# Kernel tuning notes

Measured on AMD Instinct MI355X. Metric: run time of the kernel, lower is better.

Reference implementation:

```python
import jax, jax.numpy as jnp
import numpy as np

B, T, C = 2, 1024, 2048
NH, NKV = 16, 4
HD = C // NH          # 128
NUM_REP = NH // NKV   # 4


def _apply_rotation(x, angles):
    # x: (B, T, nh, hd); angles: (T, hd//2). Equivalent to the per-pair 2x2
    # rotation matmuls in the torch code: [x0', x1'] = [[cos,-sin],[sin,cos]] @ [x0, x1]
    Bx, Tx, nh, hd = x.shape
    xp = x.reshape(Bx, Tx, nh, hd // 2, 2)
    cos = jnp.cos(angles)[None, :, None, :]  # (1, T, 1, hd//2)
    sin = jnp.sin(angles)[None, :, None, :]
    x0, x1 = xp[..., 0], xp[..., 1]
    rot = jnp.stack([cos * x0 - sin * x1, sin * x0 + cos * x1], axis=-1)
    return rot.reshape(Bx, Tx, nh, hd)


def setup_inputs() -> dict:
    key = jax.random.key(0)
    ks = jax.random.split(key, 5)
    x = jax.random.normal(ks[0], (B, T, C), dtype=jnp.float32)
    # standard RoPE angle table: pos * 10000^(-2i/hd), shape (T, hd//2)
    inv_freq = 1.0 / (10000.0 ** (jnp.arange(0, HD, 2, dtype=jnp.float32) / HD))
    angles = jnp.arange(T, dtype=jnp.float32)[:, None] * inv_freq[None, :]
    s = 0.02
    wq = jax.random.normal(ks[1], (C, C), dtype=jnp.float32) * s
    wk = jax.random.normal(ks[2], (C, NKV * HD), dtype=jnp.float32) * s
    wv = jax.random.normal(ks[3], (C, NKV * HD), dtype=jnp.float32) * s
    wo = jax.random.normal(ks[4], (C, C), dtype=jnp.float32) * s
    return {"x": x, "angles": angles, "wq": wq, "wk": wk, "wv": wv, "wo": wo}


def reference(x, angles, wq, wk, wv, wo):
    Bx, Tx, Cx = x.shape
    q = (x @ wq).reshape(Bx, Tx, NH, HD)
    k = (x @ wk).reshape(Bx, Tx, NKV, HD)
    v = (x @ wv).reshape(Bx, Tx, NKV, HD)
    q = _apply_rotation(q, angles)
    k = _apply_rotation(k, angles)
    q = q.transpose(0, 2, 1, 3)  # (B, nh, T, hd)
    k = k.transpose(0, 2, 1, 3)  # (B, nkv, T, hd)
    v = v.transpose(0, 2, 1, 3)
    if NKV != 1:
        # torch .repeat tiles kv heads: query head h uses kv head h % NKV
        k = jnp.tile(k, (1, NUM_REP, 1, 1))
        v = jnp.tile(v, (1, NUM_REP, 1, 1))
    # Faithful quirks of the source: scores = K @ Q^T (keys on rows), NO 1/sqrt(hd) scale
    scores = jnp.einsum('bhkd,bhqd->bhkq', k, q)  # (B, nh, T, T)
    mask = jnp.triu(jnp.full((Tx, Tx), -jnp.inf, dtype=scores.dtype), k=1)
    scores = scores + mask
    w = jax.nn.softmax(scores, axis=-1)
    out = jnp.einsum('bhij,bhjd->bhid', w, v)   # (B, nh, T, hd)
    out = out.transpose(0, 2, 1, 3).reshape(Bx, Tx, Cx)
    return out @ wo
```

## Files before the change

### kernel.cpp

```cpp
#include <hip/hip_runtime.h>
#include <hip/hip_bf16.h>
#include <math.h>

#define BB 2
#define TT 1024
#define CC 2048
#define NH 16
#define NKV 4
#define HD 128
#define MROWS 2048
#define QKVN 3072
#define KOFF 2048
#define VOFF 2560

typedef unsigned short u16;
typedef unsigned int   u32;
typedef _Float16 f16;
typedef _Float16 f16x8 __attribute__((ext_vector_type(8)));
typedef short    s16x8 __attribute__((ext_vector_type(8)));
typedef float    f32x4 __attribute__((ext_vector_type(4)));

__device__ __forceinline__ u16 f2h(float f) {
    union { f16 h; u16 u; } x; x.h = (f16)f; return x.u;
}
__device__ __forceinline__ float h2f(u16 u) {
    union { u16 u; f16 h; } x; x.u = u; return (float)x.h;
}

#define GLDS(gp, lp) __builtin_amdgcn_global_load_lds( \
    (const __attribute__((address_space(1))) u32*)(gp), \
    (__attribute__((address_space(3))) u32*)(lp), 16, 0, 0)

__device__ __forceinline__ void wT_tile(const float* __restrict__ src,
                                        u16* __restrict__ Wt, int Nsrc,
                                        int row_off, int idx, int t,
                                        float tile[32][33]) {
    const int k0 = (idx & 63) * 32;
    const int n0 = (idx >> 6) * 32;
    const int r = t >> 3, c4 = (t & 7) * 4;
    float4 v = *(const float4*)&src[(size_t)(k0 + r) * Nsrc + n0 + c4];
    tile[r][c4 + 0] = v.x; tile[r][c4 + 1] = v.y;
    tile[r][c4 + 2] = v.z; tile[r][c4 + 3] = v.w;
    __syncthreads();
    ushort4 o;
    o.x = f2h(tile[c4 + 0][r]); o.y = f2h(tile[c4 + 1][r]);
    o.z = f2h(tile[c4 + 2][r]); o.w = f2h(tile[c4 + 3][r]);
    *(ushort4*)&Wt[(size_t)(row_off + n0 + r) * 2048 + k0 + c4] = o;
}

__global__ __launch_bounds__(256) void prep(const float* __restrict__ x,
                                            const float* __restrict__ wq,
                                            const float* __restrict__ wk,
                                            const float* __restrict__ wv,
                                            const float* __restrict__ wo,
                                            const float* __restrict__ angles,
                                            u16* __restrict__ xb,
                                            u16* __restrict__ Wt1,
                                            u16* __restrict__ Wt2,
                                            float2* __restrict__ cs) {
    __shared__ float tile[32][33];
    const int bid = blockIdx.x, t = threadIdx.x;
    if (bid < 4096) {
        int i = bid * 256 + t;
        float4 v = ((const float4*)x)[i];
        ushort4 o;
        o.x = f2h(v.x); o.y = f2h(v.y); o.z = f2h(v.z); o.w = f2h(v.w);
        ((ushort4*)xb)[i] = o;
    } else if (bid < 8192) {
        wT_tile(wq, Wt1, 2048, 0,    bid - 4096, t, tile);
    } else if (bid < 9216) {
        wT_tile(wk, Wt1, 512,  2048, bid - 8192, t, tile);
    } else if (bid < 10240) {
        wT_tile(wv, Wt1, 512,  2560, bid - 9216, t, tile);
    } else if (bid < 14336) {
        wT_tile(wo, Wt2, 2048, 0,    bid - 10240, t, tile);
    } else {
        int i = (bid - 14336) * 256 + t;
        float a = angles[i];
        cs[i] = make_float2(cosf(a), sinf(a));
    }
}

__global__ __launch_bounds__(256) void gemm_qkv(const u16* __restrict__ A,
                                                const u16* __restrict__ Bt,
                                                u16* __restrict__ qkv,
                                                u16* __restrict__ vtg,
                                                const float2* __restrict__ cs) {
    __shared__ __align__(16) u16 As0[128 * 64];
    __shared__ __align__(16) u16 As1[128 * 64];
    __shared__ __align__(16) u16 Bs0[96 * 64];
    __shared__ __align__(16) u16 Bs1[96 * 64];
    const int t = threadIdx.x, l = t & 63, w = t >> 6;
    const int row0 = blockIdx.y * 128;
    const int col0 = blockIdx.x * 96;
    const int wr = w >> 1, wc = w & 1;
    const int lg = l >> 4, ll = l & 15;
    const int K = 2048;

    f32x4 acc[4][3] = {};

#define QSTAGE(AS, BS, k0v) do {                                              \
    _Pragma("unroll")                                                         \
    for (int e_ = 0; e_ < 4; ++e_) {                                          \
        int r_ = 32 * w + 8 * e_ + (l >> 3);                                  \
        int cg_ = (l & 7) ^ (r_ & 7);                                         \
        GLDS(A + (size_t)(row0 + r_) * K + (k0v) + cg_ * 8,                   \
             (AS) + (32 * w + 8 * e_) * 64);                                  \
    }                                                                         \
    _Pragma("unroll")                                                         \
    for (int e_ = 0; e_ < 3; ++e_) {                                          \
        int r_ = 24 * w + 8 * e_ + (l >> 3);                                  \
        int cg_ = (l & 7) ^ (r_ & 7);                                         \
        GLDS(Bt + (size_t)(col0 + r_) * K + (k0v) + cg_ * 8,                  \
             (BS) + (24 * w + 8 * e_) * 64);                                  \
    }                                                                         \
} while (0)

#define QCOMP(AS, BS) do {                                                    \
    _Pragma("unroll")                                                         \
    for (int kc_ = 0; kc_ < 2; ++kc_) {                                       \
        f16x8 af_[4], bf_[3];                                                 \
        _Pragma("unroll")                                                     \
        for (int m_ = 0; m_ < 4; ++m_) {                                      \
            int row_ = wr * 64 + 16 * m_ + ll;                                \
            af_[m_] = *(const f16x8*)&(AS)[row_ * 64 +                        \
                        (((lg + 4 * kc_) ^ (ll & 7)) * 8)];                   \
        }                                                                     \
        _Pragma("unroll")                                                     \
        for (int n_ = 0; n_ < 3; ++n_) {                                      \
            int col_ = wc * 48 + 16 * n_ + ll;                                \
            bf_[n_] = *(const f16x8*)&(BS)[col_ * 64 +                        \
                        (((lg + 4 * kc_) ^ (ll & 7)) * 8)];                   \
        }                                                                     \
        _Pragma("unroll")                                                     \
        for (int m_ = 0; m_ < 4; ++m_)                                        \
            _Pragma("unroll")                                                 \
            for (int n_ = 0; n_ < 3; ++n_)                                    \
                acc[m_][n_] = __builtin_amdgcn_mfma_f32_16x16x32_f16(         \
                    af_[m_], bf_[n_], acc[m_][n_], 0, 0, 0);                  \
    }                                                                         \
} while (0)

    QSTAGE(As0, Bs0, 0);
    __syncthreads();
#pragma unroll 1
    for (int i = 0; i < 32; i += 2) {
        QSTAGE(As1, Bs1, (i + 1) * 64);
        QCOMP(As0, Bs0);
        __syncthreads();
        if (i + 2 < 32) QSTAGE(As0, Bs0, (i + 2) * 64);
        QCOMP(As1, Bs1);
        __syncthreads();
    }
#undef QSTAGE
#undef QCOMP

    const int orow = row0 + wr * 64 + lg * 4;
    const int ocol = col0 + wc * 48 + ll;
#pragma unroll
    for (int n = 0; n < 3; ++n) {
        const int col = ocol + 16 * n;
        if (col < VOFF) {
            const int p = (col & 127) >> 1;
            const bool odd = ll & 1;
#pragma unroll
            for (int m = 0; m < 4; ++m) {
#pragma unroll
                for (int r = 0; r < 4; ++r) {
                    float v = acc[m][n][r];
                    float pr = __shfl_xor(v, 1);
                    int row = orow + 16 * m + r;
                    float2 a = cs[(row & (TT - 1)) * 64 + p];
                    float res = odd ? (a.y * pr + a.x * v) : (a.x * v - a.y * pr);
                    qkv[(size_t)row * QKVN + col] = f2h(res);
                }
            }
        } else {
            int d = col - VOFF;
            const int hk = d >> 7; d &= 127;
            const int bb = orow >> 10;
            const int base_j = orow & (TT - 1);
#pragma unroll
            for (int m = 0; m < 4; ++m) {
                ushort4 pk;
                pk.x = f2h(acc[m][n][0]); pk.y = f2h(acc[m][n][1]);
                pk.z = f2h(acc[m][n][2]); pk.w = f2h(acc[m][n][3]);
                *(ushort4*)&vtg[((size_t)(bb * NKV + hk) * 128 + d) * 1024 + base_j + 16 * m] = pk;
            }
        }
    }
}

__global__ __launch_bounds__(512) void gemm_out(const u16* __restrict__ A,
                                                const u16* __restrict__ Bt,
                                                float* __restrict__ Cf) {
    __shared__ __align__(16) u16 As0[128 * 64];
    __shared__ __align__(16) u16 As1[128 * 64];
    __shared__ __align__(16) u16 Bs0[128 * 64];
    __shared__ __align__(16) u16 Bs1[128 * 64];
    const int t = threadIdx.x, l = t & 63, w = t >> 6;
    const int row0 = blockIdx.y * 128;
    const int col0 = blockIdx.x * 128;
    const int wr = w >> 2, wc = w & 3;
    const int lg = l >> 4, ll = l & 15;
    const int K = 2048;

    f32x4 acc[4][2] = {};

#define GSTAGE(AS, BS, k0v) do {                                              \
    _Pragma("unroll")                                                         \
    for (int e_ = 0; e_ < 2; ++e_) {                                          \
        int r_ = 16 * w + 8 * e_ + (l >> 3);                                  \
        int cg_ = (l & 7) ^ (r_ & 7);                                         \
        GLDS(A  + (size_t)(row0 + r_) * K + (k0v) + cg_ * 8,                  \
             (AS) + (16 * w + 8 * e_) * 64);                                  \
        GLDS(Bt + (size_t)(col0 + r_) * K + (k0v) + cg_ * 8,                  \
             (BS) + (16 * w + 8 * e_) * 64);                                  \
    }                                                                         \
} while (0)

#define GCOMP(AS, BS) do {                                                    \
    _Pragma("unroll")                                                         \
    for (int kc_ = 0; kc_ < 2; ++kc_) {                                       \
        f16x8 af_[4], bf_[2];                                                 \
        _Pragma("unroll")                                                     \
        for (int m_ = 0; m_ < 4; ++m_) {                                      \
            int row_ = wr * 64 + 16 * m_ + ll;                                \
            af_[m_] = *(const f16x8*)&(AS)[row_ * 64 +                        \
                        (((lg + 4 * kc_) ^ (ll & 7)) * 8)];                   \
        }                                                                     \
        _Pragma("unroll")                                                     \
        for (int n_ = 0; n_ < 2; ++n_) {                                      \
            int col_ = wc * 32 + 16 * n_ + ll;                                \
            bf_[n_] = *(const f16x8*)&(BS)[col_ * 64 +                        \
                        (((lg + 4 * kc_) ^ (ll & 7)) * 8)];                   \
        }                                                                     \
        _Pragma("unroll")                                                     \
        for (int m_ = 0; m_ < 4; ++m_)                                        \
            _Pragma("unroll")                                                 \
            for (int n_ = 0; n_ < 2; ++n_)                                    \
                acc[m_][n_] = __builtin_amdgcn_mfma_f32_16x16x32_f16(         \
                    af_[m_], bf_[n_], acc[m_][n_], 0, 0, 0);                  \
    }                                                                         \
} while (0)

    GSTAGE(As0, Bs0, 0);
    __syncthreads();
#pragma unroll 1
    for (int i = 0; i < 32; i += 2) {
        GSTAGE(As1, Bs1, (i + 1) * 64);
        GCOMP(As0, Bs0);
        __syncthreads();
        if (i + 2 < 32) GSTAGE(As0, Bs0, (i + 2) * 64);
        GCOMP(As1, Bs1);
        __syncthreads();
    }
#undef GSTAGE
#undef GCOMP

    const int orow = row0 + wr * 64 + lg * 4;
    const int ocol = col0 + wc * 32 + ll;
#pragma unroll
    for (int m = 0; m < 4; ++m)
#pragma unroll
        for (int nn = 0; nn < 2; ++nn)
#pragma unroll
            for (int r = 0; r < 4; ++r)
                Cf[(size_t)(orow + 16 * m + r) * CC + ocol + 16 * nn] =
                    acc[m][nn][r];
}

__global__ __launch_bounds__(256) void attn_mfma(const u16* __restrict__ qkv,
                                                 const u16* __restrict__ vtg,
                                                 u16* __restrict__ attnb) {
    __shared__ __align__(16) u16 Qs0[64 * 128];
    __shared__ __align__(16) u16 Qs1[64 * 128];
    __shared__ __align__(16) u16 Vt0[128 * 64];
    __shared__ __align__(16) u16 Vt1[128 * 64];
    __shared__ __align__(16) u16 Ps[4 * 16 * 72];

    const int t = threadIdx.x, l = t & 63, w = t >> 6;
    const int bh = blockIdx.y;
    const int b = bh >> 4, h = bh & 15, hk = h & 3;
    const int lg = l >> 4, ll = l & 15;

    const u16* qbase = qkv + (size_t)(b * TT) * QKVN + h * 128;
    const u16* vbase = vtg + (size_t)((b * NKV + hk) * 128) * 1024;

    const int rq = 16 * w + (l >> 4);
    const int cq = l & 15;
    const int dv = 32 * w + (l >> 3);
    const int cv = l & 7;

#define STAGE(j0v, Qd, Vd) do {                                               \
    _Pragma("unroll")                                                         \
    for (int e_ = 0; e_ < 4; ++e_) {                                          \
        int r_ = rq + 4 * e_;                                                 \
        GLDS(qbase + (size_t)((j0v) + r_) * QKVN + ((cq ^ (r_ & 7)) * 8),     \
             (Qd) + (16 * w + 4 * e_) * 128);                                 \
    }                                                                         \
    _Pragma("unroll")                                                         \
    for (int e_ = 0; e_ < 4; ++e_) {                                          \
        int d_ = dv + 8 * e_;                                                 \
        GLDS(vbase + (size_t)d_ * 1024 + (j0v) + ((cv ^ (d_ & 7)) * 8),       \
             (Vd) + (32 * w + 8 * e_) * 64);                                  \
    }                                                                         \
} while (0)

#pragma unroll 1
    for (int ph = 0; ph < 2; ++ph) {
        const int it = ph ? (15 - blockIdx.x) : blockIdx.x;
        const int iw = it * 64 + w * 16;

        f16x8 kf[4];
        {
            const u16* kp = qkv + (size_t)(b * TT + iw + ll) * QKVN + KOFF + hk * 128 + lg * 8;
#pragma unroll
            for (int c = 0; c < 4; ++c) kf[c] = *(const f16x8*)(kp + 32 * c);
        }

        f32x4 o[8] = {};
        float mrun[4] = {-1e30f, -1e30f, -1e30f, -1e30f};
        float lrun[4] = {0.f, 0.f, 0.f, 0.f};

        const int nt = it + 1;
        STAGE(0, Qs0, Vt0);
        __syncthreads();

#pragma unroll 1
        for (int jt = 0; jt < nt; ++jt) {
            u16* Qc = (jt & 1) ? Qs1 : Qs0;
            u16* Vc = (jt & 1) ? Vt1 : Vt0;
            if (jt + 1 < nt) {
                u16* Qn = (jt & 1) ? Qs0 : Qs1;
                u16* Vn = (jt & 1) ? Vt0 : Vt1;
                STAGE((jt + 1) * 64, Qn, Vn);
            }

            f32x4 s[4] = {};
#pragma unroll
            for (int kc = 0; kc < 4; ++kc)
#pragma unroll
                for (int n = 0; n < 4; ++n) {
                    f16x8 qf = *(const f16x8*)&Qc[(16 * n + ll) * 128 + (((lg + 4 * kc) ^ (ll & 7)) * 8)];
                    s[n] = __builtin_amdgcn_mfma_f32_16x16x32_f16(kf[kc], qf, s[n], 0, 0, 0);
                }

            if (jt == it) {
#pragma unroll
                for (int n = 0; n < 4; ++n)
#pragma unroll
                    for (int r = 0; r < 4; ++r)
                        s[n][r] = (16 * n + ll <= 16 * w + 4 * lg + r) ? s[n][r] : -1e30f;
            }

            float tml[4];
            bool need = false;
#pragma unroll
            for (int r = 0; r < 4; ++r) {
                float tm = fmaxf(fmaxf(s[0][r], s[1][r]), fmaxf(s[2][r], s[3][r]));
                tml[r] = tm;
                need |= (tm > mrun[r] + 8.0f);
            }
            if (__any(need)) {
#pragma unroll
                for (int r = 0; r < 4; ++r) {
                    float tm = tml[r];
                    tm = fmaxf(tm, __shfl_xor(tm, 1, 16));
                    tm = fmaxf(tm, __shfl_xor(tm, 2, 16));
                    tm = fmaxf(tm, __shfl_xor(tm, 4, 16));
                    tm = fmaxf(tm, __shfl_xor(tm, 8, 16));
                    float mnew = fmaxf(mrun[r], tm);
                    float al = __expf(mrun[r] - mnew);
                    lrun[r] *= al;
                    mrun[r] = mnew;
#pragma unroll
                    for (int n = 0; n < 8; ++n) o[n][r] *= al;
                }
            }
            float p[4][4];
#pragma unroll
            for (int r = 0; r < 4; ++r) {
                float ps = 0.f;
#pragma unroll
                for (int n = 0; n < 4; ++n) { p[n][r] = __expf(s[n][r] - mrun[r]); ps += p[n][r]; }
                lrun[r] += ps;
            }

            u16* pw = Ps + w * (16 * 72);
#pragma unroll
            for (int n = 0; n < 4; ++n)
#pragma unroll
                for (int r = 0; r < 4; ++r)
                    pw[(4 * lg + r) * 72 + ll + 16 * n] = f2h(p[n][r]);
            f16x8 pa0 = *(const f16x8*)&pw[ll * 72 + 8 * lg];
            f16x8 pa1 = *(const f16x8*)&pw[ll * 72 + 8 * lg + 32];

#pragma unroll
            for (int n = 0; n < 8; ++n) {
                f16x8 vf0 = *(const f16x8*)&Vc[(16 * n + ll) * 64 + ((lg ^ (ll & 7)) * 8)];
                o[n] = __builtin_amdgcn_mfma_f32_16x16x32_f16(pa0, vf0, o[n], 0, 0, 0);
                f16x8 vf1 = *(const f16x8*)&Vc[(16 * n + ll) * 64 + (((lg + 4) ^ (ll & 7)) * 8)];
                o[n] = __builtin_amdgcn_mfma_f32_16x16x32_f16(pa1, vf1, o[n], 0, 0, 0);
            }

            __syncthreads();
        }

        u16* dst = attnb + (size_t)(b * TT + iw + 4 * lg) * CC + h * 128 + ll;
#pragma unroll
        for (int r = 0; r < 4; ++r) {
            float L = lrun[r];
            L += __shfl_xor(L, 1, 16);
            L += __shfl_xor(L, 2, 16);
            L += __shfl_xor(L, 4, 16);
            L += __shfl_xor(L, 8, 16);
            float inv = 1.0f / L;
#pragma unroll
            for (int n = 0; n < 8; ++n)
                dst[(size_t)r * CC + 16 * n] = f2h(o[n][r] * inv);
        }
    }
#undef STAGE
}

extern "C" void kernel_launch(void* const* d_in, const int* in_sizes, int n_in,
                              void* d_out, int out_size, void* d_ws, size_t ws_size,
                              hipStream_t stream) {
    const float* x      = (const float*)d_in[0];
    const float* angles = (const float*)d_in[1];
    const float* wq     = (const float*)d_in[2];
    const float* wk     = (const float*)d_in[3];
    const float* wv     = (const float*)d_in[4];
    const float* wo     = (const float*)d_in[5];
    float* out = (float*)d_out;

    char* ws = (char*)d_ws;
    u16*    Wt1   = (u16*)ws;
    u16*    Wt2   = (u16*)(ws + 12582912);
    float2* cs    = (float2*)(ws + 20971520);
    u16*    xb    = (u16*)(ws + 21495808);
    u16*    qkvb  = (u16*)(ws + 29884416);
    u16*    vtg   = (u16*)(ws + 42467328);
    u16*    attnb = (u16*)(ws + 44564480);

    prep<<<14592, 256, 0, stream>>>(x, wq, wk, wv, wo, angles, xb, Wt1, Wt2, cs);
    gemm_qkv<<<dim3(32, 16), 256, 0, stream>>>(xb, Wt1, qkvb, vtg, cs);
    attn_mfma<<<dim3(8, BB * NH), 256, 0, stream>>>(qkvb, vtg, attnb);
    gemm_out<<<dim3(16, 16), 512, 0, stream>>>(attnb, Wt2, out);
}
```

Measured before the change: 116.7 us.

## Widen QKV GEMM to 6 waves and run both causal phases concurrently in attention

The QKV GEMM goes from 4 to 6 waves per block, each computing a 64x32 sub-tile instead of 64x48, with load distribution redone across the waves. The attention kernel moves to 512 threads so that two 4-wave groups handle the paired query tiles (x and 15-x) at the same time. Previously those tiles ran in two serial phases. The groups share staged Q/V tiles, with the short group idling once its range is done. This aims to raise occupancy and latency hiding and to reuse loaded tiles, at the cost of more register pressure and idle waves in the attention loop.

```diff
diff --git a/kernel.cpp b/kernel.cpp
--- a/kernel.cpp
+++ b/kernel.cpp
@@ -81,11 +81,11 @@
     }
 }
 
-__global__ __launch_bounds__(256) void gemm_qkv(const u16* __restrict__ A,
-                                                const u16* __restrict__ Bt,
-                                                u16* __restrict__ qkv,
-                                                u16* __restrict__ vtg,
-                                                const float2* __restrict__ cs) {
+__global__ __launch_bounds__(384, 3) void gemm_qkv(const u16* __restrict__ A,
+                                                   const u16* __restrict__ Bt,
+                                                   u16* __restrict__ qkv,
+                                                   u16* __restrict__ vtg,
+                                                   const float2* __restrict__ cs) {
     __shared__ __align__(16) u16 As0[128 * 64];
     __shared__ __align__(16) u16 As1[128 * 64];
     __shared__ __align__(16) u16 Bs0[96 * 64];
@@ -93,33 +93,35 @@
     const int t = threadIdx.x, l = t & 63, w = t >> 6;
     const int row0 = blockIdx.y * 128;
     const int col0 = blockIdx.x * 96;
-    const int wr = w >> 1, wc = w & 1;
+    const int wr = w / 3, wc = w % 3;
     const int lg = l >> 4, ll = l & 15;
     const int K = 2048;
 
-    f32x4 acc[4][3] = {};
+    f32x4 acc[4][2] = {};
 
 #define QSTAGE(AS, BS, k0v) do {                                              \
     _Pragma("unroll")                                                         \
-    for (int e_ = 0; e_ < 4; ++e_) {                                          \
-        int r_ = 32 * w + 8 * e_ + (l >> 3);                                  \
-        int cg_ = (l & 7) ^ (r_ & 7);                                         \
-        GLDS(A + (size_t)(row0 + r_) * K + (k0v) + cg_ * 8,                   \
-             (AS) + (32 * w + 8 * e_) * 64);                                  \
-    }                                                                         \
-    _Pragma("unroll")                                                         \
-    for (int e_ = 0; e_ < 3; ++e_) {                                          \
-        int r_ = 24 * w + 8 * e_ + (l >> 3);                                  \
-        int cg_ = (l & 7) ^ (r_ & 7);                                         \
-        GLDS(Bt + (size_t)(col0 + r_) * K + (k0v) + cg_ * 8,                  \
-             (BS) + (24 * w + 8 * e_) * 64);                                  \
+    for (int e_ = 0; e_ < 5; ++e_) {                                          \
+        int c_ = w + 6 * e_;                                                  \
+        if (c_ < 16) {                                                        \
+            int r_ = 8 * c_ + (l >> 3);                                       \
+            GLDS(A + (size_t)(row0 + r_) * K + (k0v) +                        \
+                     (((l & 7) ^ (r_ & 7)) * 8),                              \
+                 (AS) + c_ * 512);                                            \
+        } else if (c_ < 28) {                                                 \
+            int cb_ = c_ - 16;                                                \
+            int r_ = 8 * cb_ + (l >> 3);                                      \
+            GLDS(Bt + (size_t)(col0 + r_) * K + (k0v) +                       \
+                      (((l & 7) ^ (r_ & 7)) * 8),                             \
+                 (BS) + cb_ * 512);                                           \
+        }                                                                     \
     }                                                                         \
 } while (0)
 
 #define QCOMP(AS, BS) do {                                                    \
     _Pragma("unroll")                                                         \
     for (int kc_ = 0; kc_ < 2; ++kc_) {                                       \
-        f16x8 af_[4], bf_[3];                                                 \
+        f16x8 af_[4], bf_[2];                                                 \
         _Pragma("unroll")                                                     \
         for (int m_ = 0; m_ < 4; ++m_) {                                      \
             int row_ = wr * 64 + 16 * m_ + ll;                                \
@@ -127,15 +129,15 @@
                         (((lg + 4 * kc_) ^ (ll & 7)) * 8)];                   \
         }                                                                     \
         _Pragma("unroll")                                                     \
-        for (int n_ = 0; n_ < 3; ++n_) {                                      \
-            int col_ = wc * 48 + 16 * n_ + ll;                                \
+        for (int n_ = 0; n_ < 2; ++n_) {                                      \
+            int col_ = wc * 32 + 16 * n_ + ll;                                \
             bf_[n_] = *(const f16x8*)&(BS)[col_ * 64 +                        \
                         (((lg + 4 * kc_) ^ (ll & 7)) * 8)];                   \
         }                                                                     \
         _Pragma("unroll")                                                     \
         for (int m_ = 0; m_ < 4; ++m_)                                        \
             _Pragma("unroll")                                                 \
-            for (int n_ = 0; n_ < 3; ++n_)                                    \
+            for (int n_ = 0; n_ < 2; ++n_)                                    \
                 acc[m_][n_] = __builtin_amdgcn_mfma_f32_16x16x32_f16(         \
                     af_[m_], bf_[n_], acc[m_][n_], 0, 0, 0);                  \
     }                                                                         \
@@ -156,9 +158,9 @@
 #undef QCOMP
 
     const int orow = row0 + wr * 64 + lg * 4;
-    const int ocol = col0 + wc * 48 + ll;
-#pragma unroll
-    for (int n = 0; n < 3; ++n) {
+    const int ocol = col0 + wc * 32 + ll;
+#pragma unroll
+    for (int n = 0; n < 2; ++n) {
         const int col = ocol + 16 * n;
         if (col < VOFF) {
             const int p = (col & 127) >> 1;
@@ -270,73 +272,66 @@
                     acc[m][nn][r];
 }
 
-__global__ __launch_bounds__(256) void attn_mfma(const u16* __restrict__ qkv,
-                                                 const u16* __restrict__ vtg,
-                                                 u16* __restrict__ attnb) {
+__global__ __launch_bounds__(512, 2) void attn_mfma(const u16* __restrict__ qkv,
+                                                    const u16* __restrict__ vtg,
+                                                    u16* __restrict__ attnb) {
     __shared__ __align__(16) u16 Qs0[64 * 128];
     __shared__ __align__(16) u16 Qs1[64 * 128];
     __shared__ __align__(16) u16 Vt0[128 * 64];
     __shared__ __align__(16) u16 Vt1[128 * 64];
-    __shared__ __align__(16) u16 Ps[4 * 16 * 72];
+    __shared__ __align__(16) u16 Ps[8 * 16 * 72];
 
     const int t = threadIdx.x, l = t & 63, w = t >> 6;
     const int bh = blockIdx.y;
     const int b = bh >> 4, h = bh & 15, hk = h & 3;
     const int lg = l >> 4, ll = l & 15;
+    const int wl = w & 3;
+    const int x = blockIdx.x;
+    const int myIt = (w < 4) ? x : (15 - x);
+    const int iw = myIt * 64 + wl * 16;
 
     const u16* qbase = qkv + (size_t)(b * TT) * QKVN + h * 128;
     const u16* vbase = vtg + (size_t)((b * NKV + hk) * 128) * 1024;
 
-    const int rq = 16 * w + (l >> 4);
-    const int cq = l & 15;
-    const int dv = 32 * w + (l >> 3);
-    const int cv = l & 7;
-
 #define STAGE(j0v, Qd, Vd) do {                                               \
     _Pragma("unroll")                                                         \
-    for (int e_ = 0; e_ < 4; ++e_) {                                          \
-        int r_ = rq + 4 * e_;                                                 \
-        GLDS(qbase + (size_t)((j0v) + r_) * QKVN + ((cq ^ (r_ & 7)) * 8),     \
-             (Qd) + (16 * w + 4 * e_) * 128);                                 \
-    }                                                                         \
-    _Pragma("unroll")                                                         \
-    for (int e_ = 0; e_ < 4; ++e_) {                                          \
-        int d_ = dv + 8 * e_;                                                 \
-        GLDS(vbase + (size_t)d_ * 1024 + (j0v) + ((cv ^ (d_ & 7)) * 8),       \
-             (Vd) + (32 * w + 8 * e_) * 64);                                  \
+    for (int e_ = 0; e_ < 2; ++e_) {                                          \
+        int r_ = 4 * (2 * w + e_) + (l >> 4);                                 \
+        GLDS(qbase + (size_t)((j0v) + r_) * QKVN +                            \
+                 (((l & 15) ^ (r_ & 7)) * 8),                                 \
+             (Qd) + 4 * (2 * w + e_) * 128);                                  \
+        int d_ = 8 * (2 * w + e_) + (l >> 3);                                 \
+        GLDS(vbase + (size_t)d_ * 1024 + (j0v) + (((l & 7) ^ (d_ & 7)) * 8),  \
+             (Vd) + 8 * (2 * w + e_) * 64);                                   \
     }                                                                         \
 } while (0)
 
+    f16x8 kf[4];
+    {
+        const u16* kp = qkv + (size_t)(b * TT + iw + ll) * QKVN + KOFF + hk * 128 + lg * 8;
+#pragma unroll
+        for (int c = 0; c < 4; ++c) kf[c] = *(const f16x8*)(kp + 32 * c);
+    }
+
+    f32x4 o[8] = {};
+    float mrun[4] = {-1e30f, -1e30f, -1e30f, -1e30f};
+    float lrun[4] = {0.f, 0.f, 0.f, 0.f};
+
+    const int nt = 16 - x;
+    STAGE(0, Qs0, Vt0);
+    __syncthreads();
+
 #pragma unroll 1
-    for (int ph = 0; ph < 2; ++ph) {
-        const int it = ph ? (15 - blockIdx.x) : blockIdx.x;
-        const int iw = it * 64 + w * 16;
-
-        f16x8 kf[4];
-        {
-            const u16* kp = qkv + (size_t)(b * TT + iw + ll) * QKVN + KOFF + hk * 128 + lg * 8;
-#pragma unroll
-            for (int c = 0; c < 4; ++c) kf[c] = *(const f16x8*)(kp + 32 * c);
+    for (int jt = 0; jt < nt; ++jt) {
+        u16* Qc = (jt & 1) ? Qs1 : Qs0;
+        u16* Vc = (jt & 1) ? Vt1 : Vt0;
+        if (jt + 1 < nt) {
+            u16* Qn = (jt & 1) ? Qs0 : Qs1;
+            u16* Vn = (jt & 1) ? Vt0 : Vt1;
+            STAGE((jt + 1) * 64, Qn, Vn);
         }
 
-        f32x4 o[8] = {};
-        float mrun[4] = {-1e30f, -1e30f, -1e30f, -1e30f};
-        float lrun[4] = {0.f, 0.f, 0.f, 0.f};
-
-        const int nt = it + 1;
-        STAGE(0, Qs0, Vt0);
-        __syncthreads();
-
-#pragma unroll 1
-        for (int jt = 0; jt < nt; ++jt) {
-            u16* Qc = (jt & 1) ? Qs1 : Qs0;
-            u16* Vc = (jt & 1) ? Vt1 : Vt0;
-            if (jt + 1 < nt) {
-                u16* Qn = (jt & 1) ? Qs0 : Qs1;
-                u16* Vn = (jt & 1) ? Vt0 : Vt1;
-                STAGE((jt + 1) * 64, Qn, Vn);
-            }
-
+        if (jt <= myIt) {
             f32x4 s[4] = {};
 #pragma unroll
             for (int kc = 0; kc < 4; ++kc)
@@ -346,12 +341,12 @@
                     s[n] = __builtin_amdgcn_mfma_f32_16x16x32_f16(kf[kc], qf, s[n], 0, 0, 0);
                 }
 
-            if (jt == it) {
+            if (jt == myIt) {
 #pragma unroll
                 for (int n = 0; n < 4; ++n)
 #pragma unroll
                     for (int r = 0; r < 4; ++r)
-                        s[n][r] = (16 * n + ll <= 16 * w + 4 * lg + r) ? s[n][r] : -1e30f;
+                        s[n][r] = (16 * n + ll <= 16 * wl + 4 * lg + r) ? s[n][r] : -1e30f;
             }
 
             float tml[4];
@@ -403,23 +398,23 @@
                 f16x8 vf1 = *(const f16x8*)&Vc[(16 * n + ll) * 64 + (((lg + 4) ^ (ll & 7)) * 8)];
                 o[n] = __builtin_amdgcn_mfma_f32_16x16x32_f16(pa1, vf1, o[n], 0, 0, 0);
             }
-
-            __syncthreads();
         }
 
-        u16* dst = attnb + (size_t)(b * TT + iw + 4 * lg) * CC + h * 128 + ll;
-#pragma unroll
-        for (int r = 0; r < 4; ++r) {
-            float L = lrun[r];
-            L += __shfl_xor(L, 1, 16);
-            L += __shfl_xor(L, 2, 16);
-            L += __shfl_xor(L, 4, 16);
-            L += __shfl_xor(L, 8, 16);
-            float inv = 1.0f / L;
-#pragma unroll
-            for (int n = 0; n < 8; ++n)
-                dst[(size_t)r * CC + 16 * n] = f2h(o[n][r] * inv);
-        }
+        __syncthreads();
+    }
+
+    u16* dst = attnb + (size_t)(b * TT + iw + 4 * lg) * CC + h * 128 + ll;
+#pragma unroll
+    for (int r = 0; r < 4; ++r) {
+        float L = lrun[r];
+        L += __shfl_xor(L, 1, 16);
+        L += __shfl_xor(L, 2, 16);
+        L += __shfl_xor(L, 4, 16);
+        L += __shfl_xor(L, 8, 16);
+        float inv = 1.0f / L;
+#pragma unroll
+        for (int n = 0; n < 8; ++n)
+            dst[(size_t)r * CC + 16 * n] = f2h(o[n][r] * inv);
     }
 #undef STAGE
 }
@@ -445,7 +440,7 @@
     u16*    attnb = (u16*)(ws + 44564480);
 
     prep<<<14592, 256, 0, stream>>>(x, wq, wk, wv, wo, angles, xb, Wt1, Wt2, cs);
-    gemm_qkv<<<dim3(32, 16), 256, 0, stream>>>(xb, Wt1, qkvb, vtg, cs);
-    attn_mfma<<<dim3(8, BB * NH), 256, 0, stream>>>(qkvb, vtg, attnb);
+    gemm_qkv<<<dim3(32, 16), 384, 0, stream>>>(xb, Wt1, qkvb, vtg, cs);
+    attn_mfma<<<dim3(8, BB * NH), 512, 0, stream>>>(qkvb, vtg, attnb);
     gemm_out<<<dim3(16, 16), 512, 0, stream>>>(attnb, Wt2, out);
 }
```

New measurement: 124.2 us. 1.06x slower.

## Use 32x32 MFMA in output GEMM and run paired causal tiles concurrently in attention

Applied to the files above, without the earlier changes.

The output projection GEMM now uses 32x32x16 MFMA instructions with two f32x16 accumulators instead of eight 16x16x32 tiles, which cuts LDS fragment loads per MFMA. The attention kernel now runs its two complementary causal row tiles (x and 15-x) at the same time in one 512-thread block with eight waves, instead of one after the other with four waves. Both tiles share the staged Q/V tiles, so key/value-side data is loaded once per block rather than twice, and the block has more waves to hide latency. In exchange, the waves of the shorter tile sit idle for the later iterations while still joining the barriers, and launch_bounds(512,2) may tighten the register budget.

```diff
diff --git a/kernel.cpp b/kernel.cpp
--- a/kernel.cpp
+++ b/kernel.cpp
@@ -19,6 +19,7 @@
 typedef _Float16 f16x8 __attribute__((ext_vector_type(8)));
 typedef short    s16x8 __attribute__((ext_vector_type(8)));
 typedef float    f32x4 __attribute__((ext_vector_type(4)));
+typedef float    f32x16 __attribute__((ext_vector_type(16)));
 
 __device__ __forceinline__ u16 f2h(float f) {
     union { f16 h; u16 u; } x; x.h = (f16)f; return x.u;
@@ -202,10 +203,9 @@
     const int row0 = blockIdx.y * 128;
     const int col0 = blockIdx.x * 128;
     const int wr = w >> 2, wc = w & 3;
-    const int lg = l >> 4, ll = l & 15;
     const int K = 2048;
 
-    f32x4 acc[4][2] = {};
+    f32x16 acc0 = {}, acc1 = {};
 
 #define GSTAGE(AS, BS, k0v) do {                                              \
     _Pragma("unroll")                                                         \
@@ -220,27 +220,17 @@
 } while (0)
 
 #define GCOMP(AS, BS) do {                                                    \
-    _Pragma("unroll")                                                         \
-    for (int kc_ = 0; kc_ < 2; ++kc_) {                                       \
-        f16x8 af_[4], bf_[2];                                                 \
-        _Pragma("unroll")                                                     \
-        for (int m_ = 0; m_ < 4; ++m_) {                                      \
-            int row_ = wr * 64 + 16 * m_ + ll;                                \
-            af_[m_] = *(const f16x8*)&(AS)[row_ * 64 +                        \
-                        (((lg + 4 * kc_) ^ (ll & 7)) * 8)];                   \
-        }                                                                     \
-        _Pragma("unroll")                                                     \
-        for (int n_ = 0; n_ < 2; ++n_) {                                      \
-            int col_ = wc * 32 + 16 * n_ + ll;                                \
-            bf_[n_] = *(const f16x8*)&(BS)[col_ * 64 +                        \
-                        (((lg + 4 * kc_) ^ (ll & 7)) * 8)];                   \
-        }                                                                     \
-        _Pragma("unroll")                                                     \
-        for (int m_ = 0; m_ < 4; ++m_)                                        \
-            _Pragma("unroll")                                                 \
-            for (int n_ = 0; n_ < 2; ++n_)                                    \
-                acc[m_][n_] = __builtin_amdgcn_mfma_f32_16x16x32_f16(         \
-                    af_[m_], bf_[n_], acc[m_][n_], 0, 0, 0);                  \
+    const int rA0_ = wr * 64 + (l & 31);                                      \
+    const int rA1_ = rA0_ + 32;                                               \
+    const int cB_  = wc * 32 + (l & 31);                                      \
+    _Pragma("unroll")                                                         \
+    for (int kc_ = 0; kc_ < 4; ++kc_) {                                       \
+        int c_ = 2 * kc_ + (l >> 5);                                          \
+        f16x8 af0_ = *(const f16x8*)&(AS)[rA0_ * 64 + ((c_ ^ (rA0_ & 7)) * 8)]; \
+        f16x8 af1_ = *(const f16x8*)&(AS)[rA1_ * 64 + ((c_ ^ (rA1_ & 7)) * 8)]; \
+        f16x8 bf_  = *(const f16x8*)&(BS)[cB_  * 64 + ((c_ ^ (cB_  & 7)) * 8)]; \
+        acc0 = __builtin_amdgcn_mfma_f32_32x32x16_f16(af0_, bf_, acc0, 0, 0, 0); \
+        acc1 = __builtin_amdgcn_mfma_f32_32x32x16_f16(af1_, bf_, acc1, 0, 0, 0); \
     }                                                                         \
 } while (0)
 
@@ -258,85 +248,76 @@
 #undef GSTAGE
 #undef GCOMP
 
-    const int orow = row0 + wr * 64 + lg * 4;
-    const int ocol = col0 + wc * 32 + ll;
-#pragma unroll
-    for (int m = 0; m < 4; ++m)
-#pragma unroll
-        for (int nn = 0; nn < 2; ++nn)
-#pragma unroll
-            for (int r = 0; r < 4; ++r)
-                Cf[(size_t)(orow + 16 * m + r) * CC + ocol + 16 * nn] =
-                    acc[m][nn][r];
-}
-
-__global__ __launch_bounds__(256) void attn_mfma(const u16* __restrict__ qkv,
-                                                 const u16* __restrict__ vtg,
-                                                 u16* __restrict__ attnb) {
+    const int ocol  = col0 + wc * 32 + (l & 31);
+    const int orowb = row0 + wr * 64 + 4 * (l >> 5);
+#pragma unroll
+    for (int reg = 0; reg < 16; ++reg) {
+        int row = orowb + (reg & 3) + 8 * (reg >> 2);
+        Cf[(size_t)row * CC + ocol]        = acc0[reg];
+        Cf[(size_t)(row + 32) * CC + ocol] = acc1[reg];
+    }
+}
+
+__global__ __launch_bounds__(512, 2) void attn_mfma(const u16* __restrict__ qkv,
+                                                    const u16* __restrict__ vtg,
+                                                    u16* __restrict__ attnb) {
     __shared__ __align__(16) u16 Qs0[64 * 128];
     __shared__ __align__(16) u16 Qs1[64 * 128];
     __shared__ __align__(16) u16 Vt0[128 * 64];
     __shared__ __align__(16) u16 Vt1[128 * 64];
-    __shared__ __align__(16) u16 Ps[4 * 16 * 72];
+    __shared__ __align__(16) u16 Ps[8 * 16 * 72];
 
     const int t = threadIdx.x, l = t & 63, w = t >> 6;
     const int bh = blockIdx.y;
     const int b = bh >> 4, h = bh & 15, hk = h & 3;
     const int lg = l >> 4, ll = l & 15;
+    const int wl = w & 3;
+    const int x = blockIdx.x;
+    const int myIt = (w < 4) ? x : (15 - x);
+    const int iw = myIt * 64 + wl * 16;
 
     const u16* qbase = qkv + (size_t)(b * TT) * QKVN + h * 128;
     const u16* vbase = vtg + (size_t)((b * NKV + hk) * 128) * 1024;
 
-    const int rq = 16 * w + (l >> 4);
-    const int cq = l & 15;
-    const int dv = 32 * w + (l >> 3);
-    const int cv = l & 7;
-
 #define STAGE(j0v, Qd, Vd) do {                                               \
     _Pragma("unroll")                                                         \
-    for (int e_ = 0; e_ < 4; ++e_) {                                          \
-        int r_ = rq + 4 * e_;                                                 \
-        GLDS(qbase + (size_t)((j0v) + r_) * QKVN + ((cq ^ (r_ & 7)) * 8),     \
-             (Qd) + (16 * w + 4 * e_) * 128);                                 \
-    }                                                                         \
-    _Pragma("unroll")                                                         \
-    for (int e_ = 0; e_ < 4; ++e_) {                                          \
-        int d_ = dv + 8 * e_;                                                 \
-        GLDS(vbase + (size_t)d_ * 1024 + (j0v) + ((cv ^ (d_ & 7)) * 8),       \
-             (Vd) + (32 * w + 8 * e_) * 64);                                  \
+    for (int e_ = 0; e_ < 2; ++e_) {                                          \
+        int r_ = 4 * (2 * w + e_) + (l >> 4);                                 \
+        GLDS(qbase + (size_t)((j0v) + r_) * QKVN +                            \
+                 (((l & 15) ^ (r_ & 7)) * 8),                                 \
+             (Qd) + 4 * (2 * w + e_) * 128);                                  \
+        int d_ = 8 * (2 * w + e_) + (l >> 3);                                 \
+        GLDS(vbase + (size_t)d_ * 1024 + (j0v) + (((l & 7) ^ (d_ & 7)) * 8),  \
+             (Vd) + 8 * (2 * w + e_) * 64);                                   \
     }                                                                         \
 } while (0)
 
+    f16x8 kf[4];
+    {
+        const u16* kp = qkv + (size_t)(b * TT + iw + ll) * QKVN + KOFF + hk * 128 + lg * 8;
+#pragma unroll
+        for (int c = 0; c < 4; ++c) kf[c] = *(const f16x8*)(kp + 32 * c);
+    }
+
+    f32x4 o[8] = {};
+    float mrun[4] = {-1e30f, -1e30f, -1e30f, -1e30f};
+    float lrun[4] = {0.f, 0.f, 0.f, 0.f};
+
+    const int nt = 16 - x;
+    STAGE(0, Qs0, Vt0);
+    __syncthreads();
+
 #pragma unroll 1
-    for (int ph = 0; ph < 2; ++ph) {
-        const int it = ph ? (15 - blockIdx.x) : blockIdx.x;
-        const int iw = it * 64 + w * 16;
-
-        f16x8 kf[4];
-        {
-            const u16* kp = qkv + (size_t)(b * TT + iw + ll) * QKVN + KOFF + hk * 128 + lg * 8;
-#pragma unroll
-            for (int c = 0; c < 4; ++c) kf[c] = *(const f16x8*)(kp + 32 * c);
+    for (int jt = 0; jt < nt; ++jt) {
+        u16* Qc = (jt & 1) ? Qs1 : Qs0;
+        u16* Vc = (jt & 1) ? Vt1 : Vt0;
+        if (jt + 1 < nt) {
+            u16* Qn = (jt & 1) ? Qs0 : Qs1;
+            u16* Vn = (jt & 1) ? Vt0 : Vt1;
+            STAGE((jt + 1) * 64, Qn, Vn);
         }
 
-        f32x4 o[8] = {};
-        float mrun[4] = {-1e30f, -1e30f, -1e30f, -1e30f};
-        float lrun[4] = {0.f, 0.f, 0.f, 0.f};
-
-        const int nt = it + 1;
-        STAGE(0, Qs0, Vt0);
-        __syncthreads();
-
-#pragma unroll 1
-        for (int jt = 0; jt < nt; ++jt) {
-            u16* Qc = (jt & 1) ? Qs1 : Qs0;
-            u16* Vc = (jt & 1) ? Vt1 : Vt0;
-            if (jt + 1 < nt) {
-                u16* Qn = (jt & 1) ? Qs0 : Qs1;
-                u16* Vn = (jt & 1) ? Vt0 : Vt1;
-                STAGE((jt + 1) * 64, Qn, Vn);
-            }
-
+        if (jt <= myIt) {
             f32x4 s[4] = {};
 #pragma unroll
             for (int kc = 0; kc < 4; ++kc)
@@ -346,12 +327,12 @@
                     s[n] = __builtin_amdgcn_mfma_f32_16x16x32_f16(kf[kc], qf, s[n], 0, 0, 0);
                 }
 
-            if (jt == it) {
+            if (jt == myIt) {
 #pragma unroll
                 for (int n = 0; n < 4; ++n)
 #pragma unroll
                     for (int r = 0; r < 4; ++r)
-                        s[n][r] = (16 * n + ll <= 16 * w + 4 * lg + r) ? s[n][r] : -1e30f;
+                        s[n][r] = (16 * n + ll <= 16 * wl + 4 * lg + r) ? s[n][r] : -1e30f;
             }
 
             float tml[4];
@@ -403,23 +384,23 @@
                 f16x8 vf1 = *(const f16x8*)&Vc[(16 * n + ll) * 64 + (((lg + 4) ^ (ll & 7)) * 8)];
                 o[n] = __builtin_amdgcn_mfma_f32_16x16x32_f16(pa1, vf1, o[n], 0, 0, 0);
             }
-
-            __syncthreads();
         }
 
-        u16* dst = attnb + (size_t)(b * TT + iw + 4 * lg) * CC + h * 128 + ll;
-#pragma unroll
-        for (int r = 0; r < 4; ++r) {
-            float L = lrun[r];
-            L += __shfl_xor(L, 1, 16);
-            L += __shfl_xor(L, 2, 16);
-            L += __shfl_xor(L, 4, 16);
-            L += __shfl_xor(L, 8, 16);
-            float inv = 1.0f / L;
-#pragma unroll
-            for (int n = 0; n < 8; ++n)
-                dst[(size_t)r * CC + 16 * n] = f2h(o[n][r] * inv);
-        }
+        __syncthreads();
+    }
+
+    u16* dst = attnb + (size_t)(b * TT + iw + 4 * lg) * CC + h * 128 + ll;
+#pragma unroll
+    for (int r = 0; r < 4; ++r) {
+        float L = lrun[r];
+        L += __shfl_xor(L, 1, 16);
+        L += __shfl_xor(L, 2, 16);
+        L += __shfl_xor(L, 4, 16);
+        L += __shfl_xor(L, 8, 16);
+        float inv = 1.0f / L;
+#pragma unroll
+        for (int n = 0; n < 8; ++n)
+            dst[(size_t)r * CC + 16 * n] = f2h(o[n][r] * inv);
     }
 #undef STAGE
 }
@@ -446,6 +427,6 @@
 
     prep<<<14592, 256, 0, stream>>>(x, wq, wk, wv, wo, angles, xb, Wt1, Wt2, cs);
     gemm_qkv<<<dim3(32, 16), 256, 0, stream>>>(xb, Wt1, qkvb, vtg, cs);
-    attn_mfma<<<dim3(8, BB * NH), 256, 0, stream>>>(qkvb, vtg, attnb);
+    attn_mfma<<<dim3(8, BB * NH), 512, 0, stream>>>(qkvb, vtg, attnb);
     gemm_out<<<dim3(16, 16), 512, 0, stream>>>(attnb, Wt2, out);
 }
```

Measured after the change: 113.6 us. 1.03x faster.
